# Performance work log

Hardware: AMD Instinct MI355X
Metric: run time of the kernel (lower is better)

The kernel has to match this reference:

```python
import jax, jax.numpy as jnp
import numpy as np

B, IN, H, OUT = 4096, 1024, 1024, 1024


def setup_inputs() -> dict:
    key = jax.random.key(0)
    ks = jax.random.split(key, 16)
    s_in = 1.0 / np.sqrt(IN)
    s_h = 1.0 / np.sqrt(H)
    d = {}
    d['input_vec'] = jax.random.normal(ks[0], (B, IN), jnp.float32)
    d['hidden_vec'] = jax.random.normal(ks[1], (B, H), jnp.float32)
    d['cell_vec'] = jax.random.normal(ks[2], (B, H), jnp.float32)
    names = ['f', 'i', 'o', 'g']
    for j, n in enumerate(names):
        d['Wx_' + n] = jax.random.uniform(ks[3 + 3 * j], (H, IN), jnp.float32, -s_in, s_in)
        d['bx_' + n] = jax.random.uniform(ks[4 + 3 * j], (H,), jnp.float32, -s_in, s_in)
        d['Wh_' + n] = jax.random.uniform(ks[5 + 3 * j], (H, H), jnp.float32, -s_h, s_h)
    d['W_out'] = jax.random.uniform(ks[15], (OUT, H), jnp.float32, -s_h, s_h)
    d['b_out'] = jax.random.uniform(jax.random.fold_in(key, 99), (OUT,), jnp.float32, -s_h, s_h)
    return d


def reference(input_vec, hidden_vec, cell_vec,
              Wx_f, bx_f, Wh_f,
              Wx_i, bx_i, Wh_i,
              Wx_o, bx_o, Wh_o,
              Wx_g, bx_g, Wh_g,
              W_out, b_out):
    # Fuse the 8 small linears into two GEMMs: [B,IN]x[IN,4H] and [B,H]x[H,4H].
    Wx = jnp.concatenate([Wx_f, Wx_i, Wx_o, Wx_g], axis=0)   # [4H, IN]
    Wh = jnp.concatenate([Wh_f, Wh_i, Wh_o, Wh_g], axis=0)   # [4H, H]
    b = jnp.concatenate([bx_f, bx_i, bx_o, bx_g], axis=0)    # [4H]
    gates = input_vec @ Wx.T + hidden_vec @ Wh.T + b          # [B, 4H]
    f, i, o, g = jnp.split(gates, 4, axis=1)
    f = jax.nn.sigmoid(f)
    i = jax.nn.sigmoid(i)
    o = jax.nn.sigmoid(o)
    g = jnp.tanh(g)
    new_cell = f * cell_vec + i * g
    new_hidden = o * jnp.tanh(new_cell)
    output_vec = new_hidden @ W_out.T + b_out
    return (new_hidden, new_cell, output_vec)
```

## Files before the change

### kernel.cpp

```cpp
#include <hip/hip_runtime.h>
#include <hip/hip_bf16.h>
#include <stdint.h>

#define B_   4096
#define IN_  1024
#define H_   1024
#define OUT_ 1024

typedef __attribute__((ext_vector_type(8)))  short short8;
typedef __attribute__((ext_vector_type(16))) float floatx16;

__device__ static inline void gload_lds16(const void* g, void* l) {
    __builtin_amdgcn_global_load_lds(
        (const __attribute__((address_space(1))) unsigned int*)g,
        (__attribute__((address_space(3))) unsigned int*)l,
        16, 0, 0);
}

__device__ static inline float sigmoidf_(float x) { return 1.0f / (1.0f + __expf(-x)); }
__device__ static inline float tanhf_(float x)    { return 1.0f - 2.0f / (1.0f + __expf(2.0f * x)); }

struct Ptrs8 { const float* p[8]; };

__global__ __launch_bounds__(256) void cvt_all_kernel(
        const float* __restrict__ x, const float* __restrict__ h,
        Ptrs8 ptrs, const float* __restrict__ wout,
        __hip_bfloat16* __restrict__ xh,
        __hip_bfloat16* __restrict__ Wc,
        __hip_bfloat16* __restrict__ Wob) {
    const int nth = gridDim.x * blockDim.x;
    for (int g = blockIdx.x * blockDim.x + threadIdx.x; g < 2228224; g += nth) {
        const float* src;
        __hip_bfloat16* dst;
        if (g < 1048576) {
            int b  = g >> 8;
            int c8 = (g & 255) * 8;
            src = (c8 < IN_) ? (x + (size_t)b * IN_ + c8)
                             : (h + (size_t)b * H_ + (c8 - IN_));
            dst = xh + (size_t)b * 2048 + c8;
        } else if (g < 2097152) {
            int gg = g - 1048576;
            int n  = gg >> 8;
            int c8 = (gg & 255) * 8;
            int gate = (n >> 5) & 3;
            int hh   = ((n >> 7) << 5) + (n & 31);
            src = (c8 < 1024) ? (ptrs.p[2 * gate]     + (size_t)hh * 1024 + c8)
                              : (ptrs.p[2 * gate + 1] + (size_t)hh * 1024 + (c8 - 1024));
            dst = Wc + (size_t)n * 2048 + c8;
        } else {
            int gg = g - 2097152;
            src = wout + (size_t)gg * 8;
            dst = Wob + (size_t)gg * 8;
        }
        float4 v0 = *(const float4*)src;
        float4 v1 = *(const float4*)(src + 4);
        __hip_bfloat16 tmp[8];
        tmp[0] = __float2bfloat16(v0.x);
        tmp[1] = __float2bfloat16(v0.y);
        tmp[2] = __float2bfloat16(v0.z);
        tmp[3] = __float2bfloat16(v0.w);
        tmp[4] = __float2bfloat16(v1.x);
        tmp[5] = __float2bfloat16(v1.y);
        tmp[6] = __float2bfloat16(v1.z);
        tmp[7] = __float2bfloat16(v1.w);
        *(uint4*)dst = *(const uint4*)tmp;
    }
}

__global__ __launch_bounds__(512, 2) void gemm_gate_fused(
    const __hip_bfloat16* __restrict__ A,
    const __hip_bfloat16* __restrict__ Bm,
    const float* __restrict__ cell,
    const float* __restrict__ bxf, const float* __restrict__ bxi,
    const float* __restrict__ bxo, const float* __restrict__ bxg,
    float* __restrict__ new_hidden, float* __restrict__ new_cell,
    __hip_bfloat16* __restrict__ hb)
{
    constexpr int K = 2048;

    __shared__ short sA0[16384];
    __shared__ short sB0[16384];
    __shared__ short sA1[16384];
    __shared__ short sB1[16384];

    const int tid  = threadIdx.x;
    const int lane = tid & 63;
    const int wv   = tid >> 6;
    const int wr   = wv >> 1;
    const int wc   = wv & 1;

    const int bid    = blockIdx.x;
    const int xcd    = bid & 7;
    const int loc    = bid >> 3;
    const int n_tile = xcd * 2 + (loc & 1);
    const int m_tile = loc >> 1;
    const int m0 = m_tile * 256;
    const int n0 = n_tile * 256;

    const int srow   = tid >> 3;
    const int schunk = tid & 7;
    const int scg    = schunk ^ (srow & 7);
    const __hip_bfloat16* Ag = A  + (size_t)(m0 + srow) * K + scg * 8;
    const __hip_bfloat16* Bg = Bm + (size_t)(n0 + srow) * K + scg * 8;
    const int wvoff = wv * 1024;

    const int fr    = lane & 31;
    const int khalf = lane >> 5;
    const int sw    = fr & 7;

    int offA[2], offB[4];
    #pragma unroll
    for (int i = 0; i < 2; ++i) offA[i] = (wr * 64 + i * 32 + fr) * 128;
    #pragma unroll
    for (int j = 0; j < 4; ++j) offB[j] = (wc * 128 + j * 32 + fr) * 128;

    floatx16 acc[2][4] = {};

    #pragma unroll
    for (int s = 0; s < 4; ++s)
        gload_lds16(Ag + (size_t)(s * 64) * K, (char*)sA0 + s * 8192 + wvoff);
    #pragma unroll
    for (int s = 0; s < 4; ++s)
        gload_lds16(Bg + (size_t)(s * 64) * K, (char*)sB0 + s * 8192 + wvoff);

#define TILE_BODY(RA, RB, WA, WB, tnext, DO_STAGE)                                        \
    {                                                                                     \
                         \
        __builtin_amdgcn_s_barrier();                                                     \
        if (DO_STAGE) {                                                                   \
            const __hip_bfloat16* Agt = Ag + (size_t)(tnext) * 64;                        \
            const __hip_bfloat16* Bgt = Bg + (size_t)(tnext) * 64;                        \
            _Pragma("unroll")                                                             \
            for (int s = 0; s < 4; ++s)                                                   \
                gload_lds16(Agt + (size_t)(s * 64) * K, (char*)(WA) + s * 8192 + wvoff);  \
            _Pragma("unroll")                                                             \
            for (int s = 0; s < 4; ++s)                                                   \
                gload_lds16(Bgt + (size_t)(s * 64) * K, (char*)(WB) + s * 8192 + wvoff);  \
                   \
            asm volatile("s_waitcnt vmcnt(8)" ::: "memory");                              \
        } else {                                                                          \
            asm volatile("s_waitcnt vmcnt(0)" ::: "memory");                              \
        }                                                                                 \
                              \
        __builtin_amdgcn_s_barrier();                                                     \
        __builtin_amdgcn_sched_barrier(0);                                                \
             \
        _Pragma("unroll")                                                                 \
        for (int kk = 0; kk < 4; ++kk) {                                                  \
            const int co = ((kk * 2 + khalf) ^ sw) * 16;                                  \
            short8 af[2], bfr[4];                                                         \
            _Pragma("unroll")                                                             \
            for (int i = 0; i < 2; ++i)                                                   \
                af[i]  = *(const short8*)((const char*)(RA) + offA[i] + co);              \
            _Pragma("unroll")                                                             \
            for (int j = 0; j < 4; ++j)                                                   \
                bfr[j] = *(const short8*)((const char*)(RB) + offB[j] + co);              \
            __builtin_amdgcn_s_setprio(1);                                                \
            _Pragma("unroll")                                                             \
            for (int i = 0; i < 2; ++i)                                                   \
                _Pragma("unroll")                                                         \
                for (int j = 0; j < 4; ++j)                                               \
                    acc[i][j] = __builtin_amdgcn_mfma_f32_32x32x16_bf16(                  \
                        af[i], bfr[j], acc[i][j], 0, 0, 0);                               \
            __builtin_amdgcn_s_setprio(0);                                                \
        }                                                                                 \
    }

    #pragma unroll 1
    for (int t2 = 0; t2 < 16; ++t2) {
        TILE_BODY(sA0, sB0, sA1, sB1, 2 * t2 + 1, true);
        TILE_BODY(sA1, sB1, sA0, sB0, 2 * t2 + 2, (t2 < 15));
    }
#undef TILE_BODY

    const int h  = ((n0 + wc * 128) >> 2) + fr;
    const float bfb = bxf[h];
    const float bib = bxi[h];
    const float bob = bxo[h];
    const float bgb = bxg[h];

    #pragma unroll
    for (int i = 0; i < 2; ++i) {
        const int row_base = m0 + wr * 64 + i * 32 + 4 * khalf;
        #pragma unroll
        for (int reg = 0; reg < 16; ++reg) {
            const int row = row_base + (reg & 3) + 8 * (reg >> 2);
            const size_t off = (size_t)row * H_ + h;
            const float f  = sigmoidf_(acc[i][0][reg] + bfb);
            const float ii = sigmoidf_(acc[i][1][reg] + bib);
            const float o  = sigmoidf_(acc[i][2][reg] + bob);
            const float g  = tanhf_(acc[i][3][reg] + bgb);
            const float c  = f * cell[off] + ii * g;
            const float nh = o * tanhf_(c);
            new_cell[off]   = c;
            new_hidden[off] = nh;
            hb[off] = __float2bfloat16(nh);
        }
    }
}

__global__ __launch_bounds__(256, 2) void gemm_out(
    const __hip_bfloat16* __restrict__ A,
    const __hip_bfloat16* __restrict__ Bm,
    float* __restrict__ C,
    const float* __restrict__ bias)
{
    constexpr int BK = 64;
    constexpr int K  = 1024;
    constexpr int N  = 1024;

    __shared__ __hip_bfloat16 ldsA[128 * BK];
    __shared__ __hip_bfloat16 ldsB[64 * BK];

    const int tid  = threadIdx.x;
    const int lane = tid & 63;
    const int wv   = tid >> 6;

    const int bid    = blockIdx.x;
    const int xcd    = bid & 7;
    const int loc    = bid >> 3;
    const int n_tile = xcd * 2 + (loc & 1);
    const int m_tile = loc >> 1;
    const int m0 = m_tile * 128;
    const int n0 = n_tile * 64;

    const int srow   = tid >> 3;
    const int schunk = tid & 7;
    const int scg    = schunk ^ (srow & 7);
    const __hip_bfloat16* Ag = A  + (size_t)(m0 + srow) * K + scg * 8;
    const __hip_bfloat16* Bg = Bm + (size_t)(n0 + srow) * K + scg * 8;
    char* lA = (char*)ldsA + wv * 1024;
    char* lB = (char*)ldsB + wv * 1024;

    const int wrow  = wv * 32;
    const int fr    = lane & 31;
    const int khalf = lane >> 5;

    floatx16 acc[2] = {};

    for (int k0 = 0; k0 < K; k0 += BK) {
        #pragma unroll
        for (int s = 0; s < 4; ++s)
            gload_lds16(Ag + (size_t)(s * 32) * K + k0, lA + s * 4096);
        #pragma unroll
        for (int s = 0; s < 2; ++s)
            gload_lds16(Bg + (size_t)(s * 32) * K + k0, lB + s * 4096);
        __syncthreads();

        #pragma unroll
        for (int kk = 0; kk < 4; ++kk) {
            const int cg = kk * 2 + khalf;
            const int ra = wrow + fr;
            short8 af = *(const short8*)((const char*)ldsA + ra * 128 + ((cg ^ (ra & 7)) * 16));
            short8 bf[2];
            #pragma unroll
            for (int j = 0; j < 2; ++j) {
                const int r = j * 32 + fr;
                bf[j] = *(const short8*)((const char*)ldsB + r * 128 + ((cg ^ (r & 7)) * 16));
            }
            #pragma unroll
            for (int j = 0; j < 2; ++j)
                acc[j] = __builtin_amdgcn_mfma_f32_32x32x16_bf16(af, bf[j], acc[j], 0, 0, 0);
        }
        __syncthreads();
    }

    #pragma unroll
    for (int j = 0; j < 2; ++j) {
        const int col = n0 + j * 32 + fr;
        const float bb = bias[col];
        #pragma unroll
        for (int reg = 0; reg < 16; ++reg) {
            const int row = m0 + wrow + 4 * khalf + (reg & 3) + 8 * (reg >> 2);
            C[(size_t)row * N + col] = acc[j][reg] + bb;
        }
    }
}

extern "C" void kernel_launch(void* const* d_in, const int* in_sizes, int n_in,
                              void* d_out, int out_size, void* d_ws, size_t ws_size,
                              hipStream_t stream) {
    const float* input_vec  = (const float*)d_in[0];
    const float* hidden_vec = (const float*)d_in[1];
    const float* cell_vec   = (const float*)d_in[2];
    const float* Wx_f = (const float*)d_in[3];
    const float* bx_f = (const float*)d_in[4];
    const float* Wh_f = (const float*)d_in[5];
    const float* Wx_i = (const float*)d_in[6];
    const float* bx_i = (const float*)d_in[7];
    const float* Wh_i = (const float*)d_in[8];
    const float* Wx_o = (const float*)d_in[9];
    const float* bx_o = (const float*)d_in[10];
    const float* Wh_o = (const float*)d_in[11];
    const float* Wx_g = (const float*)d_in[12];
    const float* bx_g = (const float*)d_in[13];
    const float* Wh_g = (const float*)d_in[14];
    const float* W_out = (const float*)d_in[15];
    const float* b_out = (const float*)d_in[16];

    char* ws = (char*)d_ws;
    __hip_bfloat16* xh  = (__hip_bfloat16*)(ws);
    __hip_bfloat16* Wc  = (__hip_bfloat16*)(ws + (16ull << 20));
    __hip_bfloat16* Wob = (__hip_bfloat16*)(ws + (32ull << 20));
    __hip_bfloat16* hb  = (__hip_bfloat16*)(ws + (34ull << 20));

    float* new_hidden = (float*)d_out;
    float* new_cell   = new_hidden + (size_t)B_ * H_;
    float* out_vec    = new_cell + (size_t)B_ * H_;

    Ptrs8 p;
    p.p[0] = Wx_f; p.p[1] = Wh_f; p.p[2] = Wx_i; p.p[3] = Wh_i;
    p.p[4] = Wx_o; p.p[5] = Wh_o; p.p[6] = Wx_g; p.p[7] = Wh_g;
    cvt_all_kernel<<<2048, 256, 0, stream>>>(input_vec, hidden_vec, p, W_out, xh, Wc, Wob);

    gemm_gate_fused<<<256, 512, 0, stream>>>(
        xh, Wc, cell_vec, bx_f, bx_i, bx_o, bx_g, new_hidden, new_cell, hb);

    gemm_out<<<512, 256, 0, stream>>>(hb, Wob, out_vec, b_out);
}
```

Baseline: 242.2 us.

## Double-buffer LDS tiles in output GEMM with async prefetch and manual waitcnt

Converts the gemm_out main loop from single-buffered load-then-compute into a two-stage ping-pong pipeline. The next K-tile is issued via global_load_lds into the alternate buffer while the current one is consumed, using explicit vmcnt waits and raw barriers instead of full __syncthreads, plus setprio around the MFMAs. This aims to hide global-memory latency behind the matrix math. It doubles LDS use, which may limit occupancy under the 2-block launch bound.

```diff
diff --git a/kernel.cpp b/kernel.cpp
--- a/kernel.cpp
+++ b/kernel.cpp
@@ -205,12 +205,13 @@
     float* __restrict__ C,
     const float* __restrict__ bias)
 {
-    constexpr int BK = 64;
     constexpr int K  = 1024;
     constexpr int N  = 1024;
 
-    __shared__ __hip_bfloat16 ldsA[128 * BK];
-    __shared__ __hip_bfloat16 ldsB[64 * BK];
+    __shared__ short oA0[8192];
+    __shared__ short oB0[4096];
+    __shared__ short oA1[8192];
+    __shared__ short oB1[4096];
 
     const int tid  = threadIdx.x;
     const int lane = tid & 63;
@@ -229,41 +230,68 @@
     const int scg    = schunk ^ (srow & 7);
     const __hip_bfloat16* Ag = A  + (size_t)(m0 + srow) * K + scg * 8;
     const __hip_bfloat16* Bg = Bm + (size_t)(n0 + srow) * K + scg * 8;
-    char* lA = (char*)ldsA + wv * 1024;
-    char* lB = (char*)ldsB + wv * 1024;
+    const int wvoff = wv * 1024;
 
     const int wrow  = wv * 32;
     const int fr    = lane & 31;
     const int khalf = lane >> 5;
+    const int sw    = fr & 7;
+
+    const int offA = (wrow + fr) * 128;
+    int offB[2];
+    #pragma unroll
+    for (int j = 0; j < 2; ++j) offB[j] = (j * 32 + fr) * 128;
+    const int swA = (wrow + fr) & 7;
 
     floatx16 acc[2] = {};
 
-    for (int k0 = 0; k0 < K; k0 += BK) {
-        #pragma unroll
-        for (int s = 0; s < 4; ++s)
-            gload_lds16(Ag + (size_t)(s * 32) * K + k0, lA + s * 4096);
-        #pragma unroll
-        for (int s = 0; s < 2; ++s)
-            gload_lds16(Bg + (size_t)(s * 32) * K + k0, lB + s * 4096);
-        __syncthreads();
-
-        #pragma unroll
-        for (int kk = 0; kk < 4; ++kk) {
-            const int cg = kk * 2 + khalf;
-            const int ra = wrow + fr;
-            short8 af = *(const short8*)((const char*)ldsA + ra * 128 + ((cg ^ (ra & 7)) * 16));
-            short8 bf[2];
-            #pragma unroll
-            for (int j = 0; j < 2; ++j) {
-                const int r = j * 32 + fr;
-                bf[j] = *(const short8*)((const char*)ldsB + r * 128 + ((cg ^ (r & 7)) * 16));
-            }
-            #pragma unroll
-            for (int j = 0; j < 2; ++j)
-                acc[j] = __builtin_amdgcn_mfma_f32_32x32x16_bf16(af, bf[j], acc[j], 0, 0, 0);
-        }
-        __syncthreads();
-    }
+    #pragma unroll
+    for (int s = 0; s < 4; ++s)
+        gload_lds16(Ag + (size_t)(s * 32) * K, (char*)oA0 + s * 4096 + wvoff);
+    #pragma unroll
+    for (int s = 0; s < 2; ++s)
+        gload_lds16(Bg + (size_t)(s * 32) * K, (char*)oB0 + s * 4096 + wvoff);
+
+#define OTILE_BODY(RA, RB, WA, WB, k_next, DO_STAGE)                                      \
+    {                                                                                     \
+        __builtin_amdgcn_s_barrier();                                                     \
+        if (DO_STAGE) {                                                                   \
+            _Pragma("unroll")                                                             \
+            for (int s = 0; s < 4; ++s)                                                   \
+                gload_lds16(Ag + (size_t)(s * 32) * K + (k_next),                         \
+                            (char*)(WA) + s * 4096 + wvoff);                              \
+            _Pragma("unroll")                                                             \
+            for (int s = 0; s < 2; ++s)                                                   \
+                gload_lds16(Bg + (size_t)(s * 32) * K + (k_next),                         \
+                            (char*)(WB) + s * 4096 + wvoff);                              \
+            asm volatile("s_waitcnt vmcnt(6)" ::: "memory");                              \
+        } else {                                                                          \
+            asm volatile("s_waitcnt vmcnt(0)" ::: "memory");                              \
+        }                                                                                 \
+        __builtin_amdgcn_s_barrier();                                                     \
+        __builtin_amdgcn_sched_barrier(0);                                                \
+        _Pragma("unroll")                                                                 \
+        for (int kk = 0; kk < 4; ++kk) {                                                  \
+            const int cg = kk * 2 + khalf;                                                \
+            short8 af = *(const short8*)((const char*)(RA) + offA + ((cg ^ swA) * 16));   \
+            short8 bf[2];                                                                 \
+            _Pragma("unroll")                                                             \
+            for (int j = 0; j < 2; ++j)                                                   \
+                bf[j] = *(const short8*)((const char*)(RB) + offB[j] + ((cg ^ sw) * 16)); \
+            __builtin_amdgcn_s_setprio(1);                                                \
+            _Pragma("unroll")                                                             \
+            for (int j = 0; j < 2; ++j)                                                   \
+                acc[j] = __builtin_amdgcn_mfma_f32_32x32x16_bf16(af, bf[j], acc[j], 0, 0, 0); \
+            __builtin_amdgcn_s_setprio(0);                                                \
+        }                                                                                 \
+    }
+
+    #pragma unroll 1
+    for (int t2 = 0; t2 < 8; ++t2) {
+        OTILE_BODY(oA0, oB0, oA1, oB1, (2 * t2 + 1) * 64, true);
+        OTILE_BODY(oA1, oB1, oA0, oB0, (2 * t2 + 2) * 64, (t2 < 7));
+    }
+#undef OTILE_BODY
 
     #pragma unroll
     for (int j = 0; j < 2; ++j) {
```

New measurement: 240.8 us. No clear change (-0.6%).
